# Kernel optimization log

Measured on AMD Instinct MI355X. Metric: run time of the kernel, lower is better.

The kernel has to match this reference:

```python
import jax, jax.numpy as jnp
import numpy as np

K = 3
LAMBDA_AMP = 0.1
N_NODES = 100000
N_EDGES = 1600000
D_FEAT = 50


def _proximal_l21(x, lambda_):
    # rowwise L2,1 shrinkage: scale each row by max(||row||-lambda,0)/||row||
    row_norm = jnp.linalg.norm(x, axis=1)  # [N]
    score = jnp.maximum(row_norm - lambda_, 0.0)
    score = jnp.where(row_norm > 0, score / jnp.where(row_norm > 0, row_norm, 1.0), score)
    return score[:, None] * x


def setup_inputs() -> dict:
    key = jax.random.key(0)
    k1, k2, k3, k4 = jax.random.split(key, 4)
    feat = jax.random.normal(k1, (N_NODES, D_FEAT), dtype=jnp.float32)
    edge_weight = jax.random.uniform(k2, (N_EDGES,), dtype=jnp.float32)
    src = jax.random.randint(k3, (N_EDGES,), 0, N_NODES, dtype=jnp.int32)
    dst = jax.random.randint(k4, (N_EDGES,), 0, N_NODES, dtype=jnp.int32)
    return {"feat": feat, "edge_weight": edge_weight, "src": src, "dst": dst}


def reference(feat, edge_weight, src, dst):
    n = feat.shape[0]
    # add self-loops (add_self_loop=True), self-loop weight = 1
    loop = jnp.arange(n, dtype=src.dtype)
    src_f = jnp.concatenate([src, loop])
    dst_f = jnp.concatenate([dst, loop])
    ew = jnp.concatenate([edge_weight, jnp.ones((n,), dtype=edge_weight.dtype)])

    # norm='both': w_ji = ew / (sqrt(out_deg(j)) * sqrt(in_deg(i))), weighted degrees
    out_deg = jax.ops.segment_sum(ew, src_f, num_segments=n)
    in_deg = jax.ops.segment_sum(ew, dst_f, num_segments=n)
    inv_sqrt_out = jnp.where(out_deg > 0, out_deg, 1.0) ** -0.5 * (out_deg > 0)
    inv_sqrt_in = jnp.where(in_deg > 0, in_deg, 1.0) ** -0.5 * (in_deg > 0)
    w = ew * inv_sqrt_out[src_f] * inv_sqrt_in[dst_f]  # [E+N]

    lam = LAMBDA_AMP
    gamma = 1.0 / (2.0 * (1.0 - lam))
    hh = feat
    x = feat
    for _ in range(K):
        # compute_LX: x - A_norm x  (u_mul_e + sum == SpMM over edges)
        agg = jax.ops.segment_sum(x[src_f] * w[:, None], dst_f, num_segments=n)
        lx = x - agg
        y = x - gamma * 2.0 * (1.0 - lam) * lx
        x = hh + _proximal_l21(y - hh, gamma * lam)
    return x
```

## Files before the change

### kernel.cpp

```cpp
#include <hip/hip_runtime.h>
#include <hip/hip_bf16.h>
#include <hip/hip_fp16.h>

#define D 50
#define PADH 64
#define GLAM 0.05555555555555555f
#define SCAN_B 1024
#define FIXS 8388608.0f
#define INV_FIXS (1.0f / 8388608.0f)
#define EPB 8192
#define B2T 512
#define BSH 9
#define BMSK 511u
#define BT 512
#define MAXB 256

typedef unsigned long long u64;

__global__ void k_b1(const int* __restrict__ src, const int* __restrict__ dst,
                     int* __restrict__ mat, int e, int nblk, int nbuk) {
    __shared__ unsigned hd[MAXB], hs[MAXB];
    for (int j = threadIdx.x; j < nbuk; j += blockDim.x) { hd[j] = 0; hs[j] = 0; }
    __syncthreads();
    int base = blockIdx.x * EPB;
    int end = base + EPB; if (end > e) end = e;
    for (int i = base + threadIdx.x; i < end; i += blockDim.x) {
        int t = __builtin_nontemporal_load(dst + i);
        int s = __builtin_nontemporal_load(src + i);
        atomicAdd(&hd[t >> BSH], 1u);
        atomicAdd(&hs[s >> BSH], 1u);
    }
    __syncthreads();
    for (int j = threadIdx.x; j < nbuk; j += blockDim.x) {
        mat[j * nblk + blockIdx.x] = (int)hd[j];
        mat[(nbuk + j) * nblk + blockIdx.x] = (int)hs[j];
    }
}

__global__ void k_scan1(const int* __restrict__ cnt, int* __restrict__ out,
                        int* __restrict__ bsum, int n) {
    __shared__ int s[SCAN_B];
    int i = blockIdx.x * SCAN_B + threadIdx.x;
    int v = (i < n) ? cnt[i] : 0;
    s[threadIdx.x] = v; __syncthreads();
    for (int off = 1; off < SCAN_B; off <<= 1) {
        int t = (threadIdx.x >= (unsigned)off) ? s[threadIdx.x - off] : 0;
        __syncthreads();
        s[threadIdx.x] += t; __syncthreads();
    }
    if (i < n) out[i] = s[threadIdx.x] - v;
    if (threadIdx.x == SCAN_B - 1) bsum[blockIdx.x] = s[threadIdx.x];
}

__global__ void k_scan2(int* __restrict__ bsum, int nb) {
    __shared__ int s[SCAN_B];
    int v = (threadIdx.x < (unsigned)nb) ? bsum[threadIdx.x] : 0;
    s[threadIdx.x] = v; __syncthreads();
    for (int off = 1; off < SCAN_B; off <<= 1) {
        int t = (threadIdx.x >= (unsigned)off) ? s[threadIdx.x - off] : 0;
        __syncthreads();
        s[threadIdx.x] += t; __syncthreads();
    }
    if (threadIdx.x < (unsigned)nb) bsum[threadIdx.x] = s[threadIdx.x] - v;
}

__global__ void k_scan3(int* __restrict__ out, const int* __restrict__ bsum, int n) {
    int i = blockIdx.x * SCAN_B + threadIdx.x;
    if (i < n) out[i] += bsum[blockIdx.x];
}

__global__ void k_b2(const float* __restrict__ ew, const int* __restrict__ src,
                     const int* __restrict__ dst, const int* __restrict__ msc,
                     u64* __restrict__ bind, unsigned* __restrict__ bins,
                     int e, int nblk, int nbuk) {
    __shared__ unsigned cd[MAXB], cs[MAXB];
    for (int j = threadIdx.x; j < nbuk; j += blockDim.x) {
        cd[j] = (unsigned)msc[j * nblk + blockIdx.x];
        cs[j] = (unsigned)msc[(nbuk + j) * nblk + blockIdx.x];
    }
    __syncthreads();
    int base = blockIdx.x * EPB;
    int end = base + EPB; if (end > e) end = e;
    for (int i = base + threadIdx.x; i < end; i += blockDim.x) {
        float w = __builtin_nontemporal_load(ew + i);
        int s = __builtin_nontemporal_load(src + i);
        int t = __builtin_nontemporal_load(dst + i);
        unsigned wfix = (unsigned)(w * FIXS + 0.5f);
        if (wfix > 0x7FFFFFu) wfix = 0x7FFFFFu;
        unsigned pd = atomicAdd(&cd[t >> BSH], 1u);
        bind[pd] = ((u64)__float_as_uint(w) << 32)
                 | ((unsigned)s << BSH) | (unsigned)(t & BMSK);
        unsigned ps = atomicAdd(&cs[s >> BSH], 1u);
        bins[ps - (unsigned)e] = (wfix << BSH) | (unsigned)(s & BMSK);
    }
}

__global__ void k_srcdeg(const unsigned* __restrict__ bins, const int* __restrict__ msc,
                         float* __restrict__ iso, int n, int nblk, int nbuk, int e) {
    __shared__ unsigned wl[BT];
    wl[threadIdx.x] = 0;
    __syncthreads();
    int b = blockIdx.x;
    int start = msc[(nbuk + b) * nblk] - e;
    int end = (b + 1 < nbuk) ? (msc[(nbuk + b + 1) * nblk] - e) : e;
    for (int i = start + threadIdx.x; i < end; i += blockDim.x) {
        unsigned r = bins[i];
        atomicAdd(&wl[r & BMSK], r >> BSH);
    }
    __syncthreads();
    int node = b * BT + threadIdx.x;
    if (node < n)
        iso[node] = rsqrtf(1.0f + (float)wl[threadIdx.x] * INV_FIXS);
}

__global__ void k_dstfill(const u64* __restrict__ bind, const int* __restrict__ msc,
                          const float* __restrict__ iso, float* __restrict__ isi,
                          int* __restrict__ cnt, int* __restrict__ rowptr,
                          u64* __restrict__ pe, int n, int nblk, int nbuk, int e) {
    __shared__ unsigned cl[BT], wl[BT], cur[BT];
    __shared__ int sc[BT];
    __shared__ float isL[BT];
    cl[threadIdx.x] = 0; wl[threadIdx.x] = 0;
    __syncthreads();
    int b = blockIdx.x;
    int start = msc[b * nblk];
    int end = (b + 1 < nbuk) ? msc[(b + 1) * nblk] : e;

    for (int i = start + threadIdx.x; i < end; i += blockDim.x) {
        u64 r = bind[i];
        unsigned loc = (unsigned)r & BMSK;
        float w = __uint_as_float((unsigned)(r >> 32));
        unsigned wfix = (unsigned)(w * FIXS + 0.5f);
        if (wfix > 0x7FFFFFu) wfix = 0x7FFFFFu;
        atomicAdd(&cl[loc], 1u);
        atomicAdd(&wl[loc], wfix);
    }
    __syncthreads();

    int myc = (int)cl[threadIdx.x];
    sc[threadIdx.x] = myc;
    __syncthreads();
    for (int off = 1; off < BT; off <<= 1) {
        int t = (threadIdx.x >= (unsigned)off) ? sc[threadIdx.x - off] : 0;
        __syncthreads();
        sc[threadIdx.x] += t;
        __syncthreads();
    }
    int lrp = start + sc[threadIdx.x] - myc;

    float myisi = rsqrtf(1.0f + (float)wl[threadIdx.x] * INV_FIXS);
    isL[threadIdx.x] = myisi;
    cur[threadIdx.x] = (unsigned)lrp;

    int node = b * BT + threadIdx.x;
    if (node < n) {
        isi[node] = myisi;
        cnt[node] = myc;
        rowptr[node] = lrp;
    }
    __syncthreads();

    for (int i = start + threadIdx.x; i < end; i += blockDim.x) {
        u64 r = bind[i];
        unsigned lo = (unsigned)r;
        unsigned tloc = lo & BMSK;
        unsigned s = lo >> BSH;
        float w = __uint_as_float((unsigned)(r >> 32));
        float wv = w * iso[s] * isL[tloc];
        unsigned pos = atomicAdd(&cur[tloc], 1u);
        pe[pos] = (u64)s | ((u64)__float_as_uint(wv) << 32);
    }
}

__global__ void k_pad(const float* __restrict__ feat, __half* __restrict__ xp, int n) {
    int i = blockIdx.x * blockDim.x + threadIdx.x;
    if (i < n * PADH) {
        int node = i >> 6, col = i & 63;
        xp[i] = (col < D) ? __float2half_rn(feat[node * D + col]) : __half(0.0f);
    }
}

__global__ void k_iter(const int* __restrict__ rowptr, const int* __restrict__ cnt,
                       const u64* __restrict__ pe, const __half* __restrict__ xin,
                       const float* __restrict__ feat, const float* __restrict__ iso,
                       const float* __restrict__ isi, __half* __restrict__ hout,
                       float* __restrict__ fout, int n, int final_iter) {
    int lane = threadIdx.x & 63;
    int c    = lane & 7;
    int waveId = (blockIdx.x * blockDim.x + threadIdx.x) >> 6;
    int node = waveId * 8 + (lane >> 3);
    if (node >= n) return;

    float a0 = 0.f, a1 = 0.f, a2 = 0.f, a3 = 0.f;
    float a4 = 0.f, a5 = 0.f, a6 = 0.f, a7 = 0.f;

    int beg = rowptr[node], m = cnt[node];

    int j = 0;
    for (; j + 2 <= m; j += 2) {
        u64 p0 = pe[beg + j];
        u64 p1 = pe[beg + j + 1];
        unsigned s0 = (unsigned)p0;
        float    w0 = __uint_as_float((unsigned)(p0 >> 32));
        unsigned s1 = (unsigned)p1;
        float    w1 = __uint_as_float((unsigned)(p1 >> 32));
        uint4 u0 = *(const uint4*)(xin + ((size_t)s0 << 6) + (c << 3));
        uint4 u1 = *(const uint4*)(xin + ((size_t)s1 << 6) + (c << 3));
        {
            const __half2* hp = (const __half2*)&u0;
            float2 f0 = __half22float2(hp[0]);
            float2 f1 = __half22float2(hp[1]);
            float2 f2 = __half22float2(hp[2]);
            float2 f3 = __half22float2(hp[3]);
            a0 = fmaf(w0, f0.x, a0); a1 = fmaf(w0, f0.y, a1);
            a2 = fmaf(w0, f1.x, a2); a3 = fmaf(w0, f1.y, a3);
            a4 = fmaf(w0, f2.x, a4); a5 = fmaf(w0, f2.y, a5);
            a6 = fmaf(w0, f3.x, a6); a7 = fmaf(w0, f3.y, a7);
        }
        {
            const __half2* hp = (const __half2*)&u1;
            float2 f0 = __half22float2(hp[0]);
            float2 f1 = __half22float2(hp[1]);
            float2 f2 = __half22float2(hp[2]);
            float2 f3 = __half22float2(hp[3]);
            a0 = fmaf(w1, f0.x, a0); a1 = fmaf(w1, f0.y, a1);
            a2 = fmaf(w1, f1.x, a2); a3 = fmaf(w1, f1.y, a3);
            a4 = fmaf(w1, f2.x, a4); a5 = fmaf(w1, f2.y, a5);
            a6 = fmaf(w1, f3.x, a6); a7 = fmaf(w1, f3.y, a7);
        }
    }
    if (j < m) {
        u64 p0 = pe[beg + j];
        unsigned s0 = (unsigned)p0;
        float    w0 = __uint_as_float((unsigned)(p0 >> 32));
        uint4 u0 = *(const uint4*)(xin + ((size_t)s0 << 6) + (c << 3));
        const __half2* hp = (const __half2*)&u0;
        float2 f0 = __half22float2(hp[0]);
        float2 f1 = __half22float2(hp[1]);
        float2 f2 = __half22float2(hp[2]);
        float2 f3 = __half22float2(hp[3]);
        a0 = fmaf(w0, f0.x, a0); a1 = fmaf(w0, f0.y, a1);
        a2 = fmaf(w0, f1.x, a2); a3 = fmaf(w0, f1.y, a3);
        a4 = fmaf(w0, f2.x, a4); a5 = fmaf(w0, f2.y, a5);
        a6 = fmaf(w0, f3.x, a6); a7 = fmaf(w0, f3.y, a7);
    }

    float selfw = iso[node] * isi[node];
    {
        uint4 u = *(const uint4*)(xin + ((size_t)node << 6) + (c << 3));
        const __half2* hp = (const __half2*)&u;
        float2 f0 = __half22float2(hp[0]);
        float2 f1 = __half22float2(hp[1]);
        float2 f2 = __half22float2(hp[2]);
        float2 f3 = __half22float2(hp[3]);
        a0 = fmaf(selfw, f0.x, a0); a1 = fmaf(selfw, f0.y, a1);
        a2 = fmaf(selfw, f1.x, a2); a3 = fmaf(selfw, f1.y, a3);
        a4 = fmaf(selfw, f2.x, a4); a5 = fmaf(selfw, f2.y, a5);
        a6 = fmaf(selfw, f3.x, a6); a7 = fmaf(selfw, f3.y, a7);
    }

    float f[8] = {0.f, 0.f, 0.f, 0.f, 0.f, 0.f, 0.f, 0.f};
    int fb = c << 3;
    #pragma unroll
    for (int k = 0; k < 4; ++k) {
        int ff = fb + (k << 1);
        if (ff + 1 < D) {
            float2 v = *(const float2*)(feat + (size_t)node * D + ff);
            f[k * 2] = v.x; f[k * 2 + 1] = v.y;
        }
    }

    float d0 = a0 - f[0], d1 = a1 - f[1], d2 = a2 - f[2], d3 = a3 - f[3];
    float d4 = a4 - f[4], d5 = a5 - f[5], d6 = a6 - f[6], d7 = a7 - f[7];

    float ssum = d0*d0 + d1*d1 + d2*d2 + d3*d3 + d4*d4 + d5*d5 + d6*d6 + d7*d7;
    ssum += __shfl_xor(ssum, 1, 64);
    ssum += __shfl_xor(ssum, 2, 64);
    ssum += __shfl_xor(ssum, 4, 64);
    float norm = sqrtf(ssum);
    float sc = (norm > 0.0f) ? fmaxf(norm - GLAM, 0.0f) / norm : 0.0f;

    float o0 = f[0] + sc * d0, o1 = f[1] + sc * d1;
    float o2 = f[2] + sc * d2, o3 = f[3] + sc * d3;
    float o4 = f[4] + sc * d4, o5 = f[5] + sc * d5;
    float o6 = f[6] + sc * d6, o7 = f[7] + sc * d7;
    if (!final_iter) {
        __half2 h0 = __float22half2_rn(make_float2(o0, o1));
        __half2 h1 = __float22half2_rn(make_float2(o2, o3));
        __half2 h2 = __float22half2_rn(make_float2(o4, o5));
        __half2 h3 = __float22half2_rn(make_float2(o6, o7));
        uint4 u;
        u.x = *(unsigned*)&h0; u.y = *(unsigned*)&h1;
        u.z = *(unsigned*)&h2; u.w = *(unsigned*)&h3;
        *(uint4*)(hout + ((size_t)node << 6) + (c << 3)) = u;
    } else {
        float o[8] = {o0, o1, o2, o3, o4, o5, o6, o7};
        #pragma unroll
        for (int k = 0; k < 4; ++k) {
            int ff = fb + (k << 1);
            if (ff + 1 < D) {
                float2 v; v.x = o[k * 2]; v.y = o[k * 2 + 1];
                *(float2*)(fout + (size_t)node * D + ff) = v;
            }
        }
    }
}

extern "C" void kernel_launch(void* const* d_in, const int* in_sizes, int n_in,
                              void* d_out, int out_size, void* d_ws, size_t ws_size,
                              hipStream_t stream) {
    const float* feat = (const float*)d_in[0];
    const float* ew   = (const float*)d_in[1];
    const int* src = (const int*)d_in[2];
    const int* dst = (const int*)d_in[3];

    const int nd = in_sizes[0];
    const int n  = nd / D;
    const int e  = in_sizes[1];
    const int np = n * PADH;

    const int nbuk = (n + BT - 1) / BT;
    const int nblk = (e + EPB - 1) / EPB;
    const int nm   = 2 * nbuk * nblk;

    __half*   xpA    = (__half*)d_ws;
    __half*   xpB    = xpA + np;
    u64*      bind   = (u64*)(xpB + np);
    u64*      pe     = bind + e;
    unsigned* bins   = (unsigned*)(pe + e);
    int*      mat    = (int*)(bins + e);
    int*      msc    = mat + nm;
    float*    isi    = (float*)(msc + nm);
    float*    iso    = isi + n;
    int*      cnt    = (int*)(iso + n);
    int*      rowptr = cnt + n;
    int*      bsum   = rowptr + n;
    float*    out    = (float*)d_out;

    const int B = 256;
    const int gP  = (np + B - 1) / B;
    const int NBm = (nm + SCAN_B - 1) / SCAN_B;

    k_b1<<<nblk, B2T, 0, stream>>>(src, dst, mat, e, nblk, nbuk);
    k_scan1<<<NBm, SCAN_B, 0, stream>>>(mat, msc, bsum, nm);
    k_scan2<<<1, SCAN_B, 0, stream>>>(bsum, NBm);
    k_scan3<<<NBm, SCAN_B, 0, stream>>>(msc, bsum, nm);
    k_b2<<<nblk, B2T, 0, stream>>>(ew, src, dst, msc, bind, bins, e, nblk, nbuk);
    k_srcdeg<<<nbuk, BT, 0, stream>>>(bins, msc, iso, n, nblk, nbuk, e);
    k_dstfill<<<nbuk, BT, 0, stream>>>(bind, msc, iso, isi, cnt, rowptr, pe, n, nblk, nbuk, e);
    k_pad<<<gP, B, 0, stream>>>(feat, xpA, n);

    const int nodesPerBlock = (B / 64) * 8;
    const int iterGrid = (n + nodesPerBlock - 1) / nodesPerBlock;

    k_iter<<<iterGrid, B, 0, stream>>>(rowptr, cnt, pe, xpA, feat, iso, isi, xpB, out, n, 0);
    k_iter<<<iterGrid, B, 0, stream>>>(rowptr, cnt, pe, xpB, feat, iso, isi, xpA, out, n, 0);
    k_iter<<<iterGrid, B, 0, stream>>>(rowptr, cnt, pe, xpA, feat, iso, isi, xpA, out, n, 1);
}
```

Baseline: 283.0 us.

## Stage edge scatter in LDS, fuse padding into histogram, read fp16 residual

The binning kernel now sorts each block's edges locally in shared memory: a per-block histogram and scan, then a coalesced bucket-contiguous write-out to bind/bins replaces scattered global stores. The feature padding kernel is merged into the histogram kernel as extra blocks, removing a launch. The iteration kernel reads the hh residual from a padded fp16 copy instead of fp32 feat, aligning and halving those loads at some cost in precision. k_b2 also rereads src/dst and uses large shared arrays, which lowers occupancy.

```diff
diff --git a/kernel.cpp b/kernel.cpp
--- a/kernel.cpp
+++ b/kernel.cpp
@@ -17,23 +17,32 @@
 
 typedef unsigned long long u64;
 
-__global__ void k_b1(const int* __restrict__ src, const int* __restrict__ dst,
-                     int* __restrict__ mat, int e, int nblk, int nbuk) {
-    __shared__ unsigned hd[MAXB], hs[MAXB];
-    for (int j = threadIdx.x; j < nbuk; j += blockDim.x) { hd[j] = 0; hs[j] = 0; }
-    __syncthreads();
-    int base = blockIdx.x * EPB;
-    int end = base + EPB; if (end > e) end = e;
-    for (int i = base + threadIdx.x; i < end; i += blockDim.x) {
-        int t = __builtin_nontemporal_load(dst + i);
-        int s = __builtin_nontemporal_load(src + i);
-        atomicAdd(&hd[t >> BSH], 1u);
-        atomicAdd(&hs[s >> BSH], 1u);
-    }
-    __syncthreads();
-    for (int j = threadIdx.x; j < nbuk; j += blockDim.x) {
-        mat[j * nblk + blockIdx.x] = (int)hd[j];
-        mat[(nbuk + j) * nblk + blockIdx.x] = (int)hs[j];
+__global__ void k_b1p(const int* __restrict__ src, const int* __restrict__ dst,
+                      int* __restrict__ mat, const float* __restrict__ feat,
+                      __half* __restrict__ xp, int e, int nblk, int nbuk, int n) {
+    if ((int)blockIdx.x < nblk) {
+        __shared__ unsigned hd[MAXB], hs[MAXB];
+        for (int j = threadIdx.x; j < nbuk; j += blockDim.x) { hd[j] = 0; hs[j] = 0; }
+        __syncthreads();
+        int base = blockIdx.x * EPB;
+        int end = base + EPB; if (end > e) end = e;
+        for (int i = base + threadIdx.x; i < end; i += blockDim.x) {
+            int t = __builtin_nontemporal_load(dst + i);
+            int s = __builtin_nontemporal_load(src + i);
+            atomicAdd(&hd[t >> BSH], 1u);
+            atomicAdd(&hs[s >> BSH], 1u);
+        }
+        __syncthreads();
+        for (int j = threadIdx.x; j < nbuk; j += blockDim.x) {
+            mat[j * nblk + blockIdx.x] = (int)hd[j];
+            mat[(nbuk + j) * nblk + blockIdx.x] = (int)hs[j];
+        }
+    } else {
+        int i = ((int)blockIdx.x - nblk) * (int)blockDim.x + (int)threadIdx.x;
+        if (i < n * PADH) {
+            int node = i >> 6, col = i & 63;
+            xp[i] = (col < D) ? __float2half_rn(feat[node * D + col]) : __half(0.0f);
+        }
     }
 }
 
@@ -74,24 +83,66 @@
                      u64* __restrict__ bind, unsigned* __restrict__ bins,
                      int e, int nblk, int nbuk) {
     __shared__ unsigned cd[MAXB], cs[MAXB];
-    for (int j = threadIdx.x; j < nbuk; j += blockDim.x) {
-        cd[j] = (unsigned)msc[j * nblk + blockIdx.x];
-        cs[j] = (unsigned)msc[(nbuk + j) * nblk + blockIdx.x];
-    }
+    __shared__ unsigned ld[MAXB], ls[MAXB];
+    __shared__ int gbd[MAXB], gbs[MAXB];
+    __shared__ u64 sd[EPB];
+    __shared__ unsigned ss[EPB];
+    __shared__ unsigned char bdd[EPB], bds[EPB];
+    int tid = threadIdx.x;
+    for (int j = tid; j < MAXB; j += blockDim.x) { cd[j] = 0; cs[j] = 0; }
     __syncthreads();
     int base = blockIdx.x * EPB;
     int end = base + EPB; if (end > e) end = e;
-    for (int i = base + threadIdx.x; i < end; i += blockDim.x) {
+    int m = end - base;
+
+    for (int i = base + tid; i < end; i += blockDim.x) {
+        atomicAdd(&cd[(unsigned)__builtin_nontemporal_load(dst + i) >> BSH], 1u);
+        atomicAdd(&cs[(unsigned)__builtin_nontemporal_load(src + i) >> BSH], 1u);
+    }
+    __syncthreads();
+
+    unsigned vd = 0, vs = 0;
+    if (tid < MAXB) { vd = cd[tid]; vs = cs[tid]; ld[tid] = vd; ls[tid] = vs; }
+    __syncthreads();
+    for (int off = 1; off < MAXB; off <<= 1) {
+        unsigned td = 0, ts = 0;
+        if (tid < MAXB && tid >= off) { td = ld[tid - off]; ts = ls[tid - off]; }
+        __syncthreads();
+        if (tid < MAXB) { ld[tid] += td; ls[tid] += ts; }
+        __syncthreads();
+    }
+    if (tid < MAXB) {
+        ld[tid] -= vd; ls[tid] -= vs;
+        cd[tid] = ld[tid]; cs[tid] = ls[tid];
+        if (tid < nbuk) {
+            gbd[tid] = msc[tid * nblk + blockIdx.x];
+            gbs[tid] = msc[(nbuk + tid) * nblk + blockIdx.x] - e;
+        }
+    }
+    __syncthreads();
+
+    for (int i = base + tid; i < end; i += blockDim.x) {
         float w = __builtin_nontemporal_load(ew + i);
         int s = __builtin_nontemporal_load(src + i);
         int t = __builtin_nontemporal_load(dst + i);
         unsigned wfix = (unsigned)(w * FIXS + 0.5f);
         if (wfix > 0x7FFFFFu) wfix = 0x7FFFFFu;
-        unsigned pd = atomicAdd(&cd[t >> BSH], 1u);
-        bind[pd] = ((u64)__float_as_uint(w) << 32)
-                 | ((unsigned)s << BSH) | (unsigned)(t & BMSK);
-        unsigned ps = atomicAdd(&cs[s >> BSH], 1u);
-        bins[ps - (unsigned)e] = (wfix << BSH) | (unsigned)(s & BMSK);
+        unsigned tb = (unsigned)t >> BSH, sb = (unsigned)s >> BSH;
+        unsigned pd = atomicAdd(&cd[tb], 1u);
+        sd[pd] = ((u64)__float_as_uint(w) << 32)
+               | ((unsigned)s << BSH) | (unsigned)(t & BMSK);
+        bdd[pd] = (unsigned char)tb;
+        unsigned ps = atomicAdd(&cs[sb], 1u);
+        ss[ps] = (wfix << BSH) | (unsigned)(s & BMSK);
+        bds[ps] = (unsigned char)sb;
+    }
+    __syncthreads();
+
+    for (int p = tid; p < m; p += blockDim.x) {
+        unsigned jd = bdd[p];
+        bind[gbd[jd] + (int)(p - ld[jd])] = sd[p];
+        unsigned js = bds[p];
+        bins[gbs[js] + (int)(p - ls[js])] = ss[p];
     }
 }
 
@@ -172,17 +223,9 @@
     }
 }
 
-__global__ void k_pad(const float* __restrict__ feat, __half* __restrict__ xp, int n) {
-    int i = blockIdx.x * blockDim.x + threadIdx.x;
-    if (i < n * PADH) {
-        int node = i >> 6, col = i & 63;
-        xp[i] = (col < D) ? __float2half_rn(feat[node * D + col]) : __half(0.0f);
-    }
-}
-
 __global__ void k_iter(const int* __restrict__ rowptr, const int* __restrict__ cnt,
                        const u64* __restrict__ pe, const __half* __restrict__ xin,
-                       const float* __restrict__ feat, const float* __restrict__ iso,
+                       const __half* __restrict__ xpF, const float* __restrict__ iso,
                        const float* __restrict__ isi, __half* __restrict__ hout,
                        float* __restrict__ fout, int n, int final_iter) {
     int lane = threadIdx.x & 63;
@@ -259,15 +302,16 @@
         a6 = fmaf(selfw, f3.x, a6); a7 = fmaf(selfw, f3.y, a7);
     }
 
-    float f[8] = {0.f, 0.f, 0.f, 0.f, 0.f, 0.f, 0.f, 0.f};
-    int fb = c << 3;
-    #pragma unroll
-    for (int k = 0; k < 4; ++k) {
-        int ff = fb + (k << 1);
-        if (ff + 1 < D) {
-            float2 v = *(const float2*)(feat + (size_t)node * D + ff);
-            f[k * 2] = v.x; f[k * 2 + 1] = v.y;
-        }
+    float f[8];
+    {
+        uint4 u = *(const uint4*)(xpF + ((size_t)node << 6) + (c << 3));
+        const __half2* hp = (const __half2*)&u;
+        float2 f0 = __half22float2(hp[0]);
+        float2 f1 = __half22float2(hp[1]);
+        float2 f2 = __half22float2(hp[2]);
+        float2 f3 = __half22float2(hp[3]);
+        f[0] = f0.x; f[1] = f0.y; f[2] = f1.x; f[3] = f1.y;
+        f[4] = f2.x; f[5] = f2.y; f[6] = f3.x; f[7] = f3.y;
     }
 
     float d0 = a0 - f[0], d1 = a1 - f[1], d2 = a2 - f[2], d3 = a3 - f[3];
@@ -295,6 +339,7 @@
         *(uint4*)(hout + ((size_t)node << 6) + (c << 3)) = u;
     } else {
         float o[8] = {o0, o1, o2, o3, o4, o5, o6, o7};
+        int fb = c << 3;
         #pragma unroll
         for (int k = 0; k < 4; ++k) {
             int ff = fb + (k << 1);
@@ -323,7 +368,8 @@
     const int nblk = (e + EPB - 1) / EPB;
     const int nm   = 2 * nbuk * nblk;
 
-    __half*   xpA    = (__half*)d_ws;
+    __half*   xpF    = (__half*)d_ws;
+    __half*   xpA    = xpF + np;
     __half*   xpB    = xpA + np;
     u64*      bind   = (u64*)(xpB + np);
     u64*      pe     = bind + e;
@@ -338,22 +384,21 @@
     float*    out    = (float*)d_out;
 
     const int B = 256;
-    const int gP  = (np + B - 1) / B;
+    const int gP  = (np + B2T - 1) / B2T;
     const int NBm = (nm + SCAN_B - 1) / SCAN_B;
 
-    k_b1<<<nblk, B2T, 0, stream>>>(src, dst, mat, e, nblk, nbuk);
+    k_b1p<<<nblk + gP, B2T, 0, stream>>>(src, dst, mat, feat, xpF, e, nblk, nbuk, n);
     k_scan1<<<NBm, SCAN_B, 0, stream>>>(mat, msc, bsum, nm);
     k_scan2<<<1, SCAN_B, 0, stream>>>(bsum, NBm);
     k_scan3<<<NBm, SCAN_B, 0, stream>>>(msc, bsum, nm);
     k_b2<<<nblk, B2T, 0, stream>>>(ew, src, dst, msc, bind, bins, e, nblk, nbuk);
     k_srcdeg<<<nbuk, BT, 0, stream>>>(bins, msc, iso, n, nblk, nbuk, e);
     k_dstfill<<<nbuk, BT, 0, stream>>>(bind, msc, iso, isi, cnt, rowptr, pe, n, nblk, nbuk, e);
-    k_pad<<<gP, B, 0, stream>>>(feat, xpA, n);
 
     const int nodesPerBlock = (B / 64) * 8;
     const int iterGrid = (n + nodesPerBlock - 1) / nodesPerBlock;
 
-    k_iter<<<iterGrid, B, 0, stream>>>(rowptr, cnt, pe, xpA, feat, iso, isi, xpB, out, n, 0);
-    k_iter<<<iterGrid, B, 0, stream>>>(rowptr, cnt, pe, xpB, feat, iso, isi, xpA, out, n, 0);
-    k_iter<<<iterGrid, B, 0, stream>>>(rowptr, cnt, pe, xpA, feat, iso, isi, xpA, out, n, 1);
-}
+    k_iter<<<iterGrid, B, 0, stream>>>(rowptr, cnt, pe, xpF, xpF, iso, isi, xpA, out, n, 0);
+    k_iter<<<iterGrid, B, 0, stream>>>(rowptr, cnt, pe, xpA, xpF, iso, isi, xpB, out, n, 0);
+    k_iter<<<iterGrid, B, 0, stream>>>(rowptr, cnt, pe, xpB, xpF, iso, isi, xpA, out, n, 1);
+}
```

New measurement: 271.9 us. 3.9% less time.
